# Performance work log

Hardware: AMD Instinct MI355X
Metric: run time of the kernel (lower is better)

Reference implementation:

```python
import jax, jax.numpy as jnp
import numpy as np

B, L, D, H = 64, 2048, 512, 8
DH = D // H


def setup_inputs() -> dict:
    key = jax.random.key(0)
    ks = jax.random.split(key, 8)
    Q = jax.random.normal(ks[0], (B, 1, D), dtype=jnp.float32)
    K = jax.random.normal(ks[1], (B, L, D), dtype=jnp.float32)
    s = 1.0 / np.sqrt(D)
    Ww = jax.random.uniform(ks[2], (D, D), jnp.float32, -s, s)
    Wb = jax.random.uniform(ks[3], (D,), jnp.float32, -s, s)
    Uw = jax.random.uniform(ks[4], (D, D), jnp.float32, -s, s)
    Ub = jax.random.uniform(ks[5], (D,), jnp.float32, -s, s)
    sv = 1.0 / np.sqrt(DH)
    Vw = jax.random.uniform(ks[6], (DH,), jnp.float32, -sv, sv)
    Vb = jax.random.uniform(ks[7], (1,), jnp.float32, -sv, sv)
    return {"Q": Q, "K": K, "Ww": Ww, "Wb": Wb, "Uw": Uw, "Ub": Ub, "Vw": Vw, "Vb": Vb}


def reference(Q, K, Ww, Wb, Uw, Ub, Vw, Vb):
    b, l, d = K.shape
    lq = Q.shape[1]
    # torch Linear: x @ W.T + b
    Wq = (Q @ Ww.T + Wb).reshape(b, H, lq, DH)   # raw reshape, matches torch
    Uk = (K @ Uw.T + Ub).reshape(b, H, l, DH)    # raw reshape (splits L axis)
    # V: Linear(DH -> 1) applied to tanh(W + U) -> [b, H, l]
    score = jnp.tanh(Wq + Uk) @ Vw + Vb[0]       # [b, H, l]
    score = score[:, :, None, :]                  # squeeze(-1).unsqueeze(2) -> [b, H, 1, l]
    dist = jax.nn.softmax(score, axis=-1)         # softmax over sequence
    Kh = K.reshape(b, H, l, DH)                   # raw reshape, matches torch
    attn = jnp.einsum('bhql,bhld->bhqd', dist, Kh)  # [b, H, 1, DH]
    attn = attn.reshape(b, 1, H * DH)             # [b, 1, D]
    return attn, dist
```

## Files before the change

kernel.cpp:

```cpp
#include <hip/hip_runtime.h>

typedef _Float16 h8_t __attribute__((ext_vector_type(8)));
typedef _Float16 h4_t __attribute__((ext_vector_type(4)));
typedef float f32x4 __attribute__((ext_vector_type(4)));

#define NB 64
#define NH 8
#define NL 2048
#define ND 512

__global__ __launch_bounds__(256) void wq_kernel(const float* __restrict__ Q,
                                                 const float* __restrict__ Ww,
                                                 const float* __restrict__ Wb,
                                                 float* __restrict__ Wq) {
    __shared__ float q[ND];
    const int b = blockIdx.x;
    const int t = threadIdx.x;
    for (int i = t; i < ND; i += 256) q[i] = Q[b * ND + i];
    __syncthreads();
    for (int j = t; j < ND; j += 256) {
        const float* wr = Ww + (size_t)j * ND;
        float acc = 0.f;
        for (int k = 0; k < ND; k += 4) {
            float4 w = *(const float4*)(wr + k);
            acc += q[k] * w.x + q[k + 1] * w.y + q[k + 2] * w.z + q[k + 3] * w.w;
        }
        Wq[b * ND + j] = acc + Wb[j];
    }
}

__global__ __launch_bounds__(256) void cvt_uw_kernel(const float* __restrict__ Uw,
                                                     _Float16* __restrict__ UwH) {
    const size_t i = ((size_t)blockIdx.x * 256 + threadIdx.x) * 4;
    float4 v = *(const float4*)(Uw + i);
    h4_t h = {(_Float16)v.x, (_Float16)v.y, (_Float16)v.z, (_Float16)v.w};
    *(h4_t*)(UwH + i) = h;
}

#define LDP 72

__global__ __launch_bounds__(256) void uk_score_kernel(
    const float* __restrict__ Km,
    const _Float16* __restrict__ UwH,
    const float* __restrict__ Ub,
    const float* __restrict__ Wq,
    const float* __restrict__ Vw,
    const float* __restrict__ Vb,
    float* __restrict__ scores)
{
    __shared__ _Float16 Al[128][LDP];
    __shared__ _Float16 Bl[128][LDP];

    const int t = threadIdx.x;
    const int lane = t & 63;
    const int wave = t >> 6;
    const int wm = wave >> 1;
    const int wn = wave & 1;

    const int bid = blockIdx.x;
    const int swz = (bid & 7) * 512 + (bid >> 3);
    const int tn = swz & 3;
    const int tm = swz >> 2;
    const size_t row0 = (size_t)tm * 128;
    const int n0 = tn * 128;

    f32x4 acc[4][4];
#pragma unroll
    for (int i = 0; i < 4; ++i)
#pragma unroll
        for (int j = 0; j < 4; ++j) acc[i][j] = (f32x4){0.f, 0.f, 0.f, 0.f};

    const int ar = t >> 4;
    const int ac = (t & 15) * 4;
    const int br = t >> 3;
    const int bc = (t & 7) * 8;

    for (int kk = 0; kk < ND; kk += 64) {
        const float* ga = Km + (row0 + ar) * (size_t)ND + kk + ac;
#pragma unroll
        for (int it = 0; it < 8; ++it) {
            float4 v = *(const float4*)(ga + (size_t)it * 16 * ND);
            h4_t h = {(_Float16)v.x, (_Float16)v.y, (_Float16)v.z, (_Float16)v.w};
            *(h4_t*)&Al[ar + it * 16][ac] = h;
        }
        const _Float16* gb = UwH + (size_t)(n0 + br) * ND + kk + bc;
#pragma unroll
        for (int it = 0; it < 4; ++it) {
            h8_t v = *(const h8_t*)(gb + (size_t)it * 32 * ND);
            *(h8_t*)&Bl[br + it * 32][bc] = v;
        }
        __syncthreads();
#pragma unroll
        for (int ks = 0; ks < 2; ++ks) {
            const int krd = ks * 32 + (lane >> 4) * 8;
            h8_t af[4], bf[4];
#pragma unroll
            for (int i = 0; i < 4; ++i)
                af[i] = *(const h8_t*)&Al[wm * 64 + i * 16 + (lane & 15)][krd];
#pragma unroll
            for (int j = 0; j < 4; ++j)
                bf[j] = *(const h8_t*)&Bl[wn * 64 + j * 16 + (lane & 15)][krd];
#pragma unroll
            for (int i = 0; i < 4; ++i)
#pragma unroll
                for (int j = 0; j < 4; ++j)
                    acc[i][j] = __builtin_amdgcn_mfma_f32_16x16x32_f16(af[i], bf[j], acc[i][j], 0, 0, 0);
        }
        __syncthreads();
    }

    const int b = (int)(row0 >> 11);
    const int h = ((int)row0 >> 8) & 7;
    const int i256b = (int)row0 & 255;
    const int col16 = lane & 15;

    float vw[4], wqv[4], ubv[4];
#pragma unroll
    for (int j = 0; j < 4; ++j) {
        const int jglob = n0 + wn * 64 + j * 16 + col16;
        const int dh = jglob & 63;
        vw[j] = Vw[dh];
        wqv[j] = Wq[b * ND + h * 64 + dh];
        ubv[j] = Ub[jglob];
    }
    const float vb0 = Vb[0];
    const int jb = (n0 + wn * 64) >> 6;
    const int bh = b * 8 + h;

#pragma unroll
    for (int i = 0; i < 4; ++i) {
#pragma unroll
        for (int r = 0; r < 4; ++r) {
            float s = 0.f;
#pragma unroll
            for (int j = 0; j < 4; ++j) {
                float x = acc[i][j][r] + wqv[j] + ubv[j];
                x = fminf(fmaxf(x, -15.f), 15.f);
                float e = __expf(2.f * x);
                s += ((e - 1.f) / (e + 1.f)) * vw[j];
            }
#pragma unroll
            for (int o = 8; o >= 1; o >>= 1) s += __shfl_xor(s, o);
            if (col16 == 0) {
                const int rloc = wm * 64 + i * 16 + (lane >> 4) * 4 + r;
                const int m = (i256b + rloc) * 8 + jb;
                scores[(size_t)bh * NL + m] = s + vb0;
            }
        }
    }
}

__global__ __launch_bounds__(256) void softmax_attn_kernel(
    const float* __restrict__ Km,
    const float* __restrict__ scores,
    float* __restrict__ out)
{
    __shared__ float sd[NL];
    __shared__ float red[256];
    __shared__ float att[16][64];

    const int bh = blockIdx.x;
    const int b = bh >> 3, h = bh & 7;
    const int t = threadIdx.x;

    float loc[8];
    float mx = -1e30f;
#pragma unroll
    for (int j = 0; j < 8; ++j) {
        loc[j] = scores[(size_t)bh * NL + j * 256 + t];
        mx = fmaxf(mx, loc[j]);
    }
    red[t] = mx;
    __syncthreads();
    for (int s2 = 128; s2 > 0; s2 >>= 1) {
        if (t < s2) red[t] = fmaxf(red[t], red[t + s2]);
        __syncthreads();
    }
    mx = red[0];
    __syncthreads();
    float sum = 0.f;
#pragma unroll
    for (int j = 0; j < 8; ++j) {
        loc[j] = __expf(loc[j] - mx);
        sum += loc[j];
    }
    red[t] = sum;
    __syncthreads();
    for (int s2 = 128; s2 > 0; s2 >>= 1) {
        if (t < s2) red[t] += red[t + s2];
        __syncthreads();
    }
    const float inv = 1.f / red[0];
    __syncthreads();

    float* dist_out = out + 32768 + (size_t)bh * NL;
#pragma unroll
    for (int j = 0; j < 8; ++j) {
        float d = loc[j] * inv;
        sd[j * 256 + t] = d;
        dist_out[j * 256 + t] = d;
    }
    __syncthreads();

    const int wave = t >> 6, lane = t & 63;
    const int g = lane >> 4;
    const int c4 = (lane & 15) * 4;
    f32x4 acc = (f32x4){0.f, 0.f, 0.f, 0.f};
    const float* kb = Km + ((size_t)b * NL + h * 256) * ND;
    for (int rr = 0; rr < 16; ++rr) {
        const int row = wave * 64 + rr * 4 + g;
        const float* kr = kb + (size_t)row * ND;
#pragma unroll
        for (int jb2 = 0; jb2 < 8; ++jb2) {
            const float w = sd[row * 8 + jb2];
            float4 v = *(const float4*)(kr + jb2 * 64 + c4);
            acc[0] += w * v.x;
            acc[1] += w * v.y;
            acc[2] += w * v.z;
            acc[3] += w * v.w;
        }
    }
    *(f32x4*)&att[wave * 4 + g][c4] = acc;
    __syncthreads();
    if (t < 64) {
        float a = 0.f;
#pragma unroll
        for (int i = 0; i < 16; ++i) a += att[i][t];
        out[(size_t)b * ND + h * 64 + t] = a;
    }
}

extern "C" void kernel_launch(void* const* d_in, const int* in_sizes, int n_in,
                              void* d_out, int out_size, void* d_ws, size_t ws_size,
                              hipStream_t stream) {
    const float* Q  = (const float*)d_in[0];
    const float* Km = (const float*)d_in[1];
    const float* Ww = (const float*)d_in[2];
    const float* Wb = (const float*)d_in[3];
    const float* Uw = (const float*)d_in[4];
    const float* Ub = (const float*)d_in[5];
    const float* Vw = (const float*)d_in[6];
    const float* Vb = (const float*)d_in[7];
    float* out = (float*)d_out;

    char* ws = (char*)d_ws;
    float* scores = (float*)ws;
    float* Wq = (float*)(ws + 4194304);
    _Float16* UwH = (_Float16*)(ws + 4194304 + 131072);

    wq_kernel<<<dim3(64), dim3(256), 0, stream>>>(Q, Ww, Wb, Wq);
    cvt_uw_kernel<<<dim3(256), dim3(256), 0, stream>>>(Uw, UwH);
    uk_score_kernel<<<dim3(4096), dim3(256), 0, stream>>>(Km, UwH, Ub, Wq, Vw, Vb, scores);
    softmax_attn_kernel<<<dim3(512), dim3(256), 0, stream>>>(Km, scores, out);
}
```

Before: 233.1 us.

## Widen GEMM tile to 128x256 with direct-to-LDS B loads and swizzled LDS

Restructures the Uk-score GEMM so each 512-thread block computes a 128x256 tile. Each K tile is now read once per two column halves instead of four, halving the redundant fp32 K reads and fp16 conversions. The Uw tile is loaded with global_load_lds directly into an XOR-swizzled, unpadded LDS layout, and the K step drops to 32. The K global load is issued before the barrier so its latency overlaps the LDS store. The costs are more barriers per K loop, a larger block with higher register pressure under launch_bounds(512,4), and reliance on the swizzle matching the direct-load lane mapping.

Result: faster. 191.1 us (-18.0%).

```diff
diff --git a/kernel.cpp b/kernel.cpp
--- a/kernel.cpp
+++ b/kernel.cpp
@@ -8,6 +8,14 @@
 #define NH 8
 #define NL 2048
 #define ND 512
+
+#define GLD_LDS16(g, l) \
+    __builtin_amdgcn_global_load_lds((const __attribute__((address_space(1))) unsigned int*)(g), \
+                                     (__attribute__((address_space(3))) unsigned int*)(l), 16, 0, 0)
+
+__device__ __forceinline__ int swz_idx(int row, int chunk) {
+    return row * 32 + ((chunk ^ ((row >> 1) & 3)) << 3);
+}
 
 __global__ __launch_bounds__(256) void wq_kernel(const float* __restrict__ Q,
                                                  const float* __restrict__ Ww,
@@ -37,9 +45,7 @@
     *(h4_t*)(UwH + i) = h;
 }
 
-#define LDP 72
-
-__global__ __launch_bounds__(256) void uk_score_kernel(
+__global__ __launch_bounds__(512, 4) void uk_score_kernel(
     const float* __restrict__ Km,
     const _Float16* __restrict__ UwH,
     const float* __restrict__ Ub,
@@ -48,21 +54,21 @@
     const float* __restrict__ Vb,
     float* __restrict__ scores)
 {
-    __shared__ _Float16 Al[128][LDP];
-    __shared__ _Float16 Bl[128][LDP];
+    __shared__ __align__(16) _Float16 Al[128 * 32];
+    __shared__ __align__(16) _Float16 Bl[256 * 32];
 
     const int t = threadIdx.x;
     const int lane = t & 63;
     const int wave = t >> 6;
-    const int wm = wave >> 1;
-    const int wn = wave & 1;
+    const int wm = wave >> 2;
+    const int wn = wave & 3;
 
     const int bid = blockIdx.x;
-    const int swz = (bid & 7) * 512 + (bid >> 3);
-    const int tn = swz & 3;
-    const int tm = swz >> 2;
+    const int swz = (bid & 7) * 256 + (bid >> 3);
+    const int tn = swz & 1;
+    const int tm = swz >> 1;
     const size_t row0 = (size_t)tm * 128;
-    const int n0 = tn * 128;
+    const int n0 = tn * 256;
 
     f32x4 acc[4][4];
 #pragma unroll
@@ -70,49 +76,48 @@
 #pragma unroll
         for (int j = 0; j < 4; ++j) acc[i][j] = (f32x4){0.f, 0.f, 0.f, 0.f};
 
-    const int ar = t >> 4;
-    const int ac = (t & 15) * 4;
-    const int br = t >> 3;
-    const int bc = (t & 7) * 8;
-
-    for (int kk = 0; kk < ND; kk += 64) {
-        const float* ga = Km + (row0 + ar) * (size_t)ND + kk + ac;
-#pragma unroll
-        for (int it = 0; it < 8; ++it) {
-            float4 v = *(const float4*)(ga + (size_t)it * 16 * ND);
-            h4_t h = {(_Float16)v.x, (_Float16)v.y, (_Float16)v.z, (_Float16)v.w};
-            *(h4_t*)&Al[ar + it * 16][ac] = h;
-        }
-        const _Float16* gb = UwH + (size_t)(n0 + br) * ND + kk + bc;
-#pragma unroll
-        for (int it = 0; it < 4; ++it) {
-            h8_t v = *(const h8_t*)(gb + (size_t)it * 32 * ND);
-            *(h8_t*)&Bl[br + it * 32][bc] = v;
-        }
-        __syncthreads();
-#pragma unroll
-        for (int ks = 0; ks < 2; ++ks) {
-            const int krd = ks * 32 + (lane >> 4) * 8;
-            h8_t af[4], bf[4];
-#pragma unroll
-            for (int i = 0; i < 4; ++i)
-                af[i] = *(const h8_t*)&Al[wm * 64 + i * 16 + (lane & 15)][krd];
+    const int arow = t >> 2;
+    const int achunk = t & 3;
+    const float* gA = Km + (row0 + arow) * (size_t)ND + achunk * 8;
+    _Float16* aw = &Al[swz_idx(arow, achunk)];
+
+    const int col16 = lane & 15;
+    const int kg = lane >> 4;
+
+    for (int kk = 0; kk < ND; kk += 32) {
+        const float4 v0 = *(const float4*)(gA + kk);
+        const float4 v1 = *(const float4*)(gA + kk + 4);
+        __syncthreads();
+#pragma unroll
+        for (int it = 0; it < 2; ++it) {
+            const int slot = it * 512 + t;
+            const int brow = slot >> 2;
+            const int bc = (slot & 3) ^ ((brow >> 1) & 3);
+            const _Float16* gb = UwH + (size_t)(n0 + brow) * ND + kk + bc * 8;
+            GLD_LDS16(gb, (char*)Bl + (it * 512 + (t & ~63)) * 16);
+        }
+        h8_t ah = {(_Float16)v0.x, (_Float16)v0.y, (_Float16)v0.z, (_Float16)v0.w,
+                   (_Float16)v1.x, (_Float16)v1.y, (_Float16)v1.z, (_Float16)v1.w};
+        *(h8_t*)aw = ah;
+        __syncthreads();
+
+        h8_t af[4], bf[4];
+#pragma unroll
+        for (int i = 0; i < 4; ++i)
+            af[i] = *(const h8_t*)&Al[swz_idx(wm * 64 + i * 16 + col16, kg)];
+#pragma unroll
+        for (int j = 0; j < 4; ++j)
+            bf[j] = *(const h8_t*)&Bl[swz_idx(wn * 64 + j * 16 + col16, kg)];
+#pragma unroll
+        for (int i = 0; i < 4; ++i)
 #pragma unroll
             for (int j = 0; j < 4; ++j)
-                bf[j] = *(const h8_t*)&Bl[wn * 64 + j * 16 + (lane & 15)][krd];
-#pragma unroll
-            for (int i = 0; i < 4; ++i)
-#pragma unroll
-                for (int j = 0; j < 4; ++j)
-                    acc[i][j] = __builtin_amdgcn_mfma_f32_16x16x32_f16(af[i], bf[j], acc[i][j], 0, 0, 0);
-        }
-        __syncthreads();
+                acc[i][j] = __builtin_amdgcn_mfma_f32_16x16x32_f16(af[i], bf[j], acc[i][j], 0, 0, 0);
     }
 
     const int b = (int)(row0 >> 11);
     const int h = ((int)row0 >> 8) & 7;
     const int i256b = (int)row0 & 255;
-    const int col16 = lane & 15;
 
     float vw[4], wqv[4], ubv[4];
 #pragma unroll
@@ -124,7 +129,7 @@
         ubv[j] = Ub[jglob];
     }
     const float vb0 = Vb[0];
-    const int jb = (n0 + wn * 64) >> 6;
+    const int jb = tn * 4 + wn;
     const int bh = b * 8 + h;
 
 #pragma unroll
@@ -250,6 +255,6 @@
 
     wq_kernel<<<dim3(64), dim3(256), 0, stream>>>(Q, Ww, Wb, Wq);
     cvt_uw_kernel<<<dim3(256), dim3(256), 0, stream>>>(Uw, UwH);
-    uk_score_kernel<<<dim3(4096), dim3(256), 0, stream>>>(Km, UwH, Ub, Wq, Vw, Vb, scores);
+    uk_score_kernel<<<dim3(2048), dim3(512), 0, stream>>>(Km, UwH, Ub, Wq, Vw, Vb, scores);
     softmax_attn_kernel<<<dim3(512), dim3(256), 0, stream>>>(Km, scores, out);
 }
```

## Software-pipeline UK GEMM with register prefetch, swizzled LDS A tile, direct B loads

Applied to the files above, without the earlier changes.

The K·Uw^T MFMA main loop is restructured into 16 steps of 32-wide K slices. Each step prefetches the next A slice into alternating register buffers and loads the B (UwH) fragments straight from global memory into registers, so B no longer goes through LDS. The A tile uses a smaller XOR-swizzled LDS layout instead of padded rows, with sched_barriers and setprio to overlap global loads with MFMA work. launch_bounds is raised to target 3 blocks per CU, which risks register pressure, and the B loads from global are uncoalesced per-lane row reads.

Result: slower. 264.5 us (+13.5%).

```diff
diff --git a/kernel.cpp b/kernel.cpp
--- a/kernel.cpp
+++ b/kernel.cpp
@@ -8,6 +8,12 @@
 #define NH 8
 #define NL 2048
 #define ND 512
+
+#define SBAR() __builtin_amdgcn_sched_barrier(0)
+
+__device__ __forceinline__ int swz_idx(int row, int chunk) {
+    return row * 32 + ((chunk ^ ((row >> 1) & 3)) << 3);
+}
 
 __global__ __launch_bounds__(256) void wq_kernel(const float* __restrict__ Q,
                                                  const float* __restrict__ Ww,
@@ -37,9 +43,7 @@
     *(h4_t*)(UwH + i) = h;
 }
 
-#define LDP 72
-
-__global__ __launch_bounds__(256) void uk_score_kernel(
+__global__ __launch_bounds__(256, 3) void uk_score_kernel(
     const float* __restrict__ Km,
     const _Float16* __restrict__ UwH,
     const float* __restrict__ Ub,
@@ -48,14 +52,15 @@
     const float* __restrict__ Vb,
     float* __restrict__ scores)
 {
-    __shared__ _Float16 Al[128][LDP];
-    __shared__ _Float16 Bl[128][LDP];
+    __shared__ __align__(16) _Float16 Al[128 * 32];
 
     const int t = threadIdx.x;
     const int lane = t & 63;
     const int wave = t >> 6;
     const int wm = wave >> 1;
     const int wn = wave & 1;
+    const int col16 = lane & 15;
+    const int kg = lane >> 4;
 
     const int bid = blockIdx.x;
     const int swz = (bid & 7) * 512 + (bid >> 3);
@@ -64,55 +69,101 @@
     const size_t row0 = (size_t)tm * 128;
     const int n0 = tn * 128;
 
+    const int arow = t >> 1;
+    const int ah = t & 1;
+    const float* gA = Km + (row0 + arow) * (size_t)ND + ah * 16;
+    const int adst0 = swz_idx(arow, ah * 2);
+    const int adst1 = swz_idx(arow, ah * 2 + 1);
+
+    const _Float16* gB[4];
+#pragma unroll
+    for (int j = 0; j < 4; ++j)
+        gB[j] = UwH + (size_t)(n0 + wn * 64 + j * 16 + col16) * ND + kg * 8;
+
     f32x4 acc[4][4];
 #pragma unroll
     for (int i = 0; i < 4; ++i)
 #pragma unroll
         for (int j = 0; j < 4; ++j) acc[i][j] = (f32x4){0.f, 0.f, 0.f, 0.f};
 
-    const int ar = t >> 4;
-    const int ac = (t & 15) * 4;
-    const int br = t >> 3;
-    const int bc = (t & 7) * 8;
-
-    for (int kk = 0; kk < ND; kk += 64) {
-        const float* ga = Km + (row0 + ar) * (size_t)ND + kk + ac;
-#pragma unroll
-        for (int it = 0; it < 8; ++it) {
-            float4 v = *(const float4*)(ga + (size_t)it * 16 * ND);
-            h4_t h = {(_Float16)v.x, (_Float16)v.y, (_Float16)v.z, (_Float16)v.w};
-            *(h4_t*)&Al[ar + it * 16][ac] = h;
-        }
-        const _Float16* gb = UwH + (size_t)(n0 + br) * ND + kk + bc;
-#pragma unroll
-        for (int it = 0; it < 4; ++it) {
-            h8_t v = *(const h8_t*)(gb + (size_t)it * 32 * ND);
-            *(h8_t*)&Bl[br + it * 32][bc] = v;
-        }
-        __syncthreads();
-#pragma unroll
-        for (int ks = 0; ks < 2; ++ks) {
-            const int krd = ks * 32 + (lane >> 4) * 8;
-            h8_t af[4], bf[4];
-#pragma unroll
-            for (int i = 0; i < 4; ++i)
-                af[i] = *(const h8_t*)&Al[wm * 64 + i * 16 + (lane & 15)][krd];
+    float4 ra0[4], ra1[4];
+    h8_t bf[4];
+
+#pragma unroll
+    for (int q = 0; q < 4; ++q) ra0[q] = *(const float4*)(gA + q * 4);
+#pragma unroll
+    for (int q = 0; q < 4; ++q) ra1[q] = *(const float4*)(gA + 32 + q * 4);
+#pragma unroll
+    for (int j = 0; j < 4; ++j) bf[j] = *(const h8_t*)(gB[j]);
+    {
+        h8_t h0 = {(_Float16)ra0[0].x, (_Float16)ra0[0].y, (_Float16)ra0[0].z, (_Float16)ra0[0].w,
+                   (_Float16)ra0[1].x, (_Float16)ra0[1].y, (_Float16)ra0[1].z, (_Float16)ra0[1].w};
+        h8_t h1 = {(_Float16)ra0[2].x, (_Float16)ra0[2].y, (_Float16)ra0[2].z, (_Float16)ra0[2].w,
+                   (_Float16)ra0[3].x, (_Float16)ra0[3].y, (_Float16)ra0[3].z, (_Float16)ra0[3].w};
+        *(h8_t*)&Al[adst0] = h0;
+        *(h8_t*)&Al[adst1] = h1;
+    }
+
+#pragma unroll
+    for (int s = 0; s < 16; ++s) {
+        asm volatile("s_waitcnt lgkmcnt(0)" ::: "memory");
+        SBAR();
+        __builtin_amdgcn_s_barrier();
+        SBAR();
+        if (s <= 13) {
+            if (s & 1) {
+#pragma unroll
+                for (int q = 0; q < 4; ++q) ra1[q] = *(const float4*)(gA + (s + 2) * 32 + q * 4);
+            } else {
+#pragma unroll
+                for (int q = 0; q < 4; ++q) ra0[q] = *(const float4*)(gA + (s + 2) * 32 + q * 4);
+            }
+        }
+        SBAR();
+        h8_t af[4];
+#pragma unroll
+        for (int i = 0; i < 4; ++i)
+            af[i] = *(const h8_t*)&Al[swz_idx(wm * 64 + i * 16 + col16, kg)];
+        asm volatile("s_waitcnt lgkmcnt(0)" ::: "memory");
+        SBAR();
+        __builtin_amdgcn_s_setprio(1);
+#pragma unroll
+        for (int i = 0; i < 4; ++i)
 #pragma unroll
             for (int j = 0; j < 4; ++j)
-                bf[j] = *(const h8_t*)&Bl[wn * 64 + j * 16 + (lane & 15)][krd];
-#pragma unroll
-            for (int i = 0; i < 4; ++i)
-#pragma unroll
-                for (int j = 0; j < 4; ++j)
-                    acc[i][j] = __builtin_amdgcn_mfma_f32_16x16x32_f16(af[i], bf[j], acc[i][j], 0, 0, 0);
-        }
-        __syncthreads();
+                acc[i][j] = __builtin_amdgcn_mfma_f32_16x16x32_f16(af[i], bf[j], acc[i][j], 0, 0, 0);
+        __builtin_amdgcn_s_setprio(0);
+        SBAR();
+        if (s <= 14) {
+#pragma unroll
+            for (int j = 0; j < 4; ++j) bf[j] = *(const h8_t*)(gB[j] + (s + 1) * 32);
+        }
+        SBAR();
+        if (s <= 14) {
+            __builtin_amdgcn_s_barrier();
+            SBAR();
+            if (s & 1) {
+                h8_t h0 = {(_Float16)ra0[0].x, (_Float16)ra0[0].y, (_Float16)ra0[0].z, (_Float16)ra0[0].w,
+                           (_Float16)ra0[1].x, (_Float16)ra0[1].y, (_Float16)ra0[1].z, (_Float16)ra0[1].w};
+                h8_t h1 = {(_Float16)ra0[2].x, (_Float16)ra0[2].y, (_Float16)ra0[2].z, (_Float16)ra0[2].w,
+                           (_Float16)ra0[3].x, (_Float16)ra0[3].y, (_Float16)ra0[3].z, (_Float16)ra0[3].w};
+                *(h8_t*)&Al[adst0] = h0;
+                *(h8_t*)&Al[adst1] = h1;
+            } else {
+                h8_t h0 = {(_Float16)ra1[0].x, (_Float16)ra1[0].y, (_Float16)ra1[0].z, (_Float16)ra1[0].w,
+                           (_Float16)ra1[1].x, (_Float16)ra1[1].y, (_Float16)ra1[1].z, (_Float16)ra1[1].w};
+                h8_t h1 = {(_Float16)ra1[2].x, (_Float16)ra1[2].y, (_Float16)ra1[2].z, (_Float16)ra1[2].w,
+                           (_Float16)ra1[3].x, (_Float16)ra1[3].y, (_Float16)ra1[3].z, (_Float16)ra1[3].w};
+                *(h8_t*)&Al[adst0] = h0;
+                *(h8_t*)&Al[adst1] = h1;
+            }
+            SBAR();
+        }
     }
 
     const int b = (int)(row0 >> 11);
     const int h = ((int)row0 >> 8) & 7;
     const int i256b = (int)row0 & 255;
-    const int col16 = lane & 15;
 
     float vw[4], wqv[4], ubv[4];
 #pragma unroll
@@ -124,7 +175,7 @@
         ubv[j] = Ub[jglob];
     }
     const float vb0 = Vb[0];
-    const int jb = (n0 + wn * 64) >> 6;
+    const int jb = tn * 2 + wn;
     const int bh = b * 8 + h;
 
 #pragma unroll
@@ -142,7 +193,7 @@
 #pragma unroll
             for (int o = 8; o >= 1; o >>= 1) s += __shfl_xor(s, o);
             if (col16 == 0) {
-                const int rloc = wm * 64 + i * 16 + (lane >> 4) * 4 + r;
+                const int rloc = wm * 64 + i * 16 + kg * 4 + r;
                 const int m = (i256b + rloc) * 8 + jb;
                 scores[(size_t)bh * NL + m] = s + vb0;
             }
```
